# Kernel optimization log

Measured on AMD Instinct MI355X. Metric: run time of the kernel, lower is better.

The kernel has to match this reference:

```python
import jax, jax.numpy as jnp
import numpy as np

N, D, C, TOPK = 4096, 512, 512, 5


def setup_inputs() -> dict:
    key = jax.random.key(0)
    k1, k2, k3, k4 = jax.random.split(key, 4)
    feat1 = jax.random.normal(k1, (N, D), dtype=jnp.float32)
    feat2 = jax.random.normal(k2, (N, D), dtype=jnp.float32)
    # probs are softmax outputs in the original pipeline -> valid BCE inputs in (0,1)
    prob1 = jax.nn.softmax(jax.random.normal(k3, (N, C), dtype=jnp.float32), axis=-1)
    prob2 = jax.nn.softmax(jax.random.normal(k4, (N, C), dtype=jnp.float32), axis=-1)
    return {"feat1": feat1, "feat2": feat2, "prob1": prob1, "prob2": prob2, "topk": TOPK}


def reference(feat1, feat2, prob1, prob2, topk):
    # rank statistics on detached feat1: top-k feature indices, sorted as a set
    rank_idx = jnp.argsort(-feat1, axis=1)           # descending argsort, (N, D)
    top = jnp.sort(rank_idx[:, :topk], axis=1)       # (N, K) sorted top-k index sets
    # pair_enum layout: pair k = j*N + i with x1 -> row i (fast), x2 -> row j (slow).
    # Build the equivalent (N, N) matrices with rows=j, cols=i.
    rank_diff = jnp.abs(top[None, :, :] - top[:, None, :]).sum(-1)  # (N, N)
    target = (rank_diff == 0).astype(prob1.dtype)
    # pred_sim[k] = dot(prob1[i], prob2[j])  ->  P[j, i]
    pred_sim = prob2 @ prob1.T                        # (N, N)
    # BCELoss with torch's log clamp at -100
    log_p = jnp.clip(jnp.log(pred_sim), -100.0)
    log_1mp = jnp.clip(jnp.log(1.0 - pred_sim), -100.0)
    loss = -jnp.mean(target * log_p + (1.0 - target) * log_1mp)
    return loss
```

## Files before the change

### kernel.cpp

```cpp
#include <hip/hip_runtime.h>
#include <hip/hip_bf16.h>
#include <stdint.h>

#define NROWS 4096
#define CDIM  512
#define TOPK  5
#define BMJ   128
#define BNI   256
#define BK    32
#define NKT   16

typedef __bf16 bf16x8 __attribute__((ext_vector_type(8)));
typedef float  f32x4  __attribute__((ext_vector_type(4)));
typedef unsigned long long u64;

__global__ __launch_bounds__(256) void
prep_kernel(const float* __restrict__ p1, const float* __restrict__ p2,
            const float* __restrict__ feat1,
            __bf16* __restrict__ o1, __bf16* __restrict__ o2,
            u64* __restrict__ keys) {
  const int bid = blockIdx.x, tid = threadIdx.x;
  if (bid < 2048) {
    const int arr = bid >> 10;
    const int b2  = bid & 1023;
    const int kt  = b2 >> 6;
    const int c   = (b2 & 63) * 256 + tid;
    const int row = c >> 2;
    const int s   = c & 3;
    const float* src = (arr ? p2 : p1) + (size_t)row * CDIM + kt * 32 + s * 8;
    __bf16*      dst = (arr ? o2 : o1) + ((size_t)kt * NROWS + row) * 32 + ((s ^ (row & 3)) * 8);
    const float4 a = *(const float4*)src;
    const float4 b = *(const float4*)(src + 4);
    bf16x8 v;
    v[0]=(__bf16)a.x; v[1]=(__bf16)a.y; v[2]=(__bf16)a.z; v[3]=(__bf16)a.w;
    v[4]=(__bf16)b.x; v[5]=(__bf16)b.y; v[6]=(__bf16)b.z; v[7]=(__bf16)b.w;
    *(bf16x8*)dst = v;
  } else {
    const int row = (bid - 2048) * 4 + (tid >> 6);
    const int l   = tid & 63;
    const float* r = feat1 + (size_t)row * CDIM;
    float v[8];
    const float4 a = *(const float4*)(r + l * 8);
    const float4 b = *(const float4*)(r + l * 8 + 4);
    v[0]=a.x; v[1]=a.y; v[2]=a.z; v[3]=a.w;
    v[4]=b.x; v[5]=b.y; v[6]=b.z; v[7]=b.w;

    int sel[TOPK];
#pragma unroll
    for (int s = 0; s < TOPK; ++s) {
      float bv = -__builtin_inff();
      int   bi = 0x7fffffff;
#pragma unroll
      for (int t = 0; t < 8; ++t)
        if (v[t] > bv) { bv = v[t]; bi = l * 8 + t; }
#pragma unroll
      for (int off = 32; off > 0; off >>= 1) {
        float ov = __shfl_xor(bv, off);
        int   oi = __shfl_xor(bi, off);
        if (ov > bv || (ov == bv && oi < bi)) { bv = ov; bi = oi; }
      }
      sel[s] = bi;
      const int loc = bi - l * 8;
      if (loc >= 0 && loc < 8) v[loc] = -__builtin_inff();
    }
#define CSWAP(x, y) { int mn = min(sel[x], sel[y]); int mx = max(sel[x], sel[y]); sel[x] = mn; sel[y] = mx; }
    CSWAP(0,1) CSWAP(3,4) CSWAP(2,4) CSWAP(2,3) CSWAP(1,4)
    CSWAP(0,3) CSWAP(0,2) CSWAP(1,3) CSWAP(1,2)
#undef CSWAP
    if (l == 0) {
      keys[row] = (u64)sel[0] | ((u64)sel[1] << 9) | ((u64)sel[2] << 18)
                | ((u64)sel[3] << 27) | ((u64)sel[4] << 36);
    }
  }
}

__global__ __launch_bounds__(512, 4) void
gemm_loss_kernel(const __bf16* __restrict__ o1k,
                 const __bf16* __restrict__ o2k,
                 const u64* __restrict__ keys,
                 float* __restrict__ partials) {
  __shared__ __bf16 smA[3][BMJ * BK];
  __shared__ __bf16 smB[3][BNI * BK];
  __shared__ float  red[512];

  const int tid = threadIdx.x;
  const int l   = tid & 63, w = tid >> 6;
  const int wr  = w >> 2,  wc = w & 3;
  const int lr  = l & 15,  kq = l >> 4;

  const int bid = blockIdx.x;
  const int x   = bid & 7, v = bid >> 3;
  const int jt  = (x & 3) * 8 + (v & 7);
  const int it  = (x >> 2) * 8 + (v >> 3);
  const int jb  = jt * BMJ, ib = it * BNI;

  f32x4 acc[4][4] = {};

  const __bf16* gA0 = o2k + (size_t)jb * 32;
  const __bf16* gB0 = o1k + (size_t)ib * 32;

  auto stage = [&](int slot, int kt) {
    const size_t ko = (size_t)kt * NROWS * 32;
    __builtin_amdgcn_global_load_lds(
        (const __attribute__((address_space(1))) unsigned int*)(const void*)(gA0 + ko + tid * 8),
        (__attribute__((address_space(3))) unsigned int*)(void*)&smA[slot][w * 512], 16, 0, 0);
#pragma unroll
    for (int i = 0; i < 2; ++i) {
      __builtin_amdgcn_global_load_lds(
          (const __attribute__((address_space(1))) unsigned int*)(const void*)(gB0 + ko + (i * 512 + tid) * 8),
          (__attribute__((address_space(3))) unsigned int*)(void*)&smB[slot][i * 4096 + w * 512], 16, 0, 0);
    }
  };

  auto compute = [&](int slot) {
    bf16x8 af[4], bfr[4];
#pragma unroll
    for (int m = 0; m < 4; ++m) {
      const int r = wr * 64 + m * 16 + lr;
      const int p = kq ^ (r & 3);
      af[m] = *(const bf16x8*)&smA[slot][r * 32 + p * 8];
    }
#pragma unroll
    for (int n = 0; n < 4; ++n) {
      const int r = wc * 64 + n * 16 + lr;
      const int p = kq ^ (r & 3);
      bfr[n] = *(const bf16x8*)&smB[slot][r * 32 + p * 8];
    }
    __builtin_amdgcn_s_setprio(1);
#pragma unroll
    for (int m = 0; m < 4; ++m)
#pragma unroll
      for (int n = 0; n < 4; ++n)
        acc[m][n] = __builtin_amdgcn_mfma_f32_16x16x32_bf16(af[m], bfr[n], acc[m][n], 0, 0, 0);
    __builtin_amdgcn_s_setprio(0);
  };

  stage(0, 0);
  stage(1, 1);
  for (int kt = 0; kt < NKT; ++kt) {
    if (kt == NKT - 1) asm volatile("s_waitcnt vmcnt(0)" ::: "memory");
    else               asm volatile("s_waitcnt vmcnt(3)" ::: "memory");
    __builtin_amdgcn_s_barrier();
    __builtin_amdgcn_sched_barrier(0);
    if (kt + 2 < NKT) stage((kt + 2) % 3, kt + 2);
    compute(kt % 3);
  }

  u64 ki[4];
#pragma unroll
  for (int n = 0; n < 4; ++n)
    ki[n] = keys[ib + wc * 64 + n * 16 + lr];

  float sum = 0.f;
#pragma unroll
  for (int m = 0; m < 4; ++m)
#pragma unroll
    for (int r = 0; r < 4; ++r) {
      const u64 kj = keys[jb + wr * 64 + m * 16 + kq * 4 + r];
#pragma unroll
      for (int n = 0; n < 4; ++n) {
        const float p = acc[m][n][r];
        const bool  t = (kj == ki[n]);
        const float xx = t ? p : (1.0f - p);
        sum += fmaxf(__logf(xx), -100.0f);
      }
    }

  red[tid] = sum;
  __syncthreads();
#pragma unroll
  for (int s = 256; s > 0; s >>= 1) {
    if (tid < s) red[tid] += red[tid + s];
    __syncthreads();
  }
  if (tid == 0) partials[bid] = red[0];
}

__global__ void finalize_kernel(const float* __restrict__ partials,
                                float* __restrict__ out) {
  __shared__ float red[256];
  red[threadIdx.x] = partials[threadIdx.x] + partials[threadIdx.x + 256];
  __syncthreads();
  for (int st = 128; st > 0; st >>= 1) {
    if (threadIdx.x < st) red[threadIdx.x] += red[threadIdx.x + st];
    __syncthreads();
  }
  if (threadIdx.x == 0) out[0] = -red[0] * (1.0f / 16777216.0f);
}

extern "C" void kernel_launch(void* const* d_in, const int* in_sizes, int n_in,
                              void* d_out, int out_size, void* d_ws, size_t ws_size,
                              hipStream_t stream) {
  (void)in_sizes; (void)n_in; (void)out_size; (void)ws_size;
  const float* feat1 = (const float*)d_in[0];
  const float* prob1 = (const float*)d_in[2];
  const float* prob2 = (const float*)d_in[3];

  __bf16* o1 = (__bf16*)d_ws;
  __bf16* o2 = (__bf16*)((char*)d_ws + (size_t)NROWS * CDIM * 2);
  u64*   keys = (u64*)((char*)d_ws + (size_t)NROWS * CDIM * 4);
  float* partials = (float*)((char*)d_ws + (size_t)NROWS * CDIM * 4 + NROWS * 8);

  prep_kernel<<<3072, 256, 0, stream>>>(prob1, prob2, feat1, o1, o2, keys);
  gemm_loss_kernel<<<512, 512, 0, stream>>>(o1, o2, keys, partials);
  finalize_kernel<<<1, 256, 0, stream>>>(partials, (float*)d_out);
}
```

Measured before the change: 40.13 us.

## Enlarge GEMM tile to 256x256 with 4-stage split-phase pipeline

Grows the output tile per block from 128x256 to 256x256, halving the grid to 256 blocks so each block gets more reuse per loaded K-slice. The K loop becomes two half-phases, with the A and B prefetches interleaved between MFMA groups across a 4-slot LDS ring. The LDS swizzle is changed to mix higher row bits. The trade-off is twice the accumulator registers, occupancy cut to 2 blocks per CU, and only 256 blocks on a 256-CU device, which risks a single under-filled wave.

```diff
diff --git a/kernel.cpp b/kernel.cpp
--- a/kernel.cpp
+++ b/kernel.cpp
@@ -5,14 +5,15 @@
 #define NROWS 4096
 #define CDIM  512
 #define TOPK  5
-#define BMJ   128
-#define BNI   256
+#define BT    256
 #define BK    32
 #define NKT   16
 
 typedef __bf16 bf16x8 __attribute__((ext_vector_type(8)));
 typedef float  f32x4  __attribute__((ext_vector_type(4)));
 typedef unsigned long long u64;
+
+__device__ __forceinline__ int swz(int row) { return (row ^ (row >> 2)) & 3; }
 
 __global__ __launch_bounds__(256) void
 prep_kernel(const float* __restrict__ p1, const float* __restrict__ p2,
@@ -28,7 +29,7 @@
     const int row = c >> 2;
     const int s   = c & 3;
     const float* src = (arr ? p2 : p1) + (size_t)row * CDIM + kt * 32 + s * 8;
-    __bf16*      dst = (arr ? o2 : o1) + ((size_t)kt * NROWS + row) * 32 + ((s ^ (row & 3)) * 8);
+    __bf16*      dst = (arr ? o2 : o1) + ((size_t)kt * NROWS + row) * 32 + ((s ^ swz(row)) * 8);
     const float4 a = *(const float4*)src;
     const float4 b = *(const float4*)(src + 4);
     bf16x8 v;
@@ -74,13 +75,13 @@
   }
 }
 
-__global__ __launch_bounds__(512, 4) void
+__global__ __launch_bounds__(512, 2) void
 gemm_loss_kernel(const __bf16* __restrict__ o1k,
                  const __bf16* __restrict__ o2k,
                  const u64* __restrict__ keys,
                  float* __restrict__ partials) {
-  __shared__ __bf16 smA[3][BMJ * BK];
-  __shared__ __bf16 smB[3][BNI * BK];
+  __shared__ __bf16 smA[4][BT * BK];
+  __shared__ __bf16 smB[4][BT * BK];
   __shared__ float  red[512];
 
   const int tid = threadIdx.x;
@@ -89,61 +90,85 @@
   const int lr  = l & 15,  kq = l >> 4;
 
   const int bid = blockIdx.x;
-  const int x   = bid & 7, v = bid >> 3;
-  const int jt  = (x & 3) * 8 + (v & 7);
-  const int it  = (x >> 2) * 8 + (v >> 3);
-  const int jb  = jt * BMJ, ib = it * BNI;
-
-  f32x4 acc[4][4] = {};
-
-  const __bf16* gA0 = o2k + (size_t)jb * 32;
-  const __bf16* gB0 = o1k + (size_t)ib * 32;
-
-  auto stage = [&](int slot, int kt) {
-    const size_t ko = (size_t)kt * NROWS * 32;
-    __builtin_amdgcn_global_load_lds(
-        (const __attribute__((address_space(1))) unsigned int*)(const void*)(gA0 + ko + tid * 8),
-        (__attribute__((address_space(3))) unsigned int*)(void*)&smA[slot][w * 512], 16, 0, 0);
-#pragma unroll
-    for (int i = 0; i < 2; ++i) {
+  const int x   = bid & 7, bv = bid >> 3;
+  const int jt  = (x & 3) * 4 + (bv & 3);
+  const int it  = (x >> 2) * 8 + (bv >> 2);
+  const int jb  = jt * BT, ib = it * BT;
+
+  f32x4 acc[8][4] = {};
+
+  auto stageA = [&](int slot, int kt) {
+    const size_t ko = (size_t)kt * NROWS * 32 + (size_t)jb * 32;
+#pragma unroll
+    for (int r = 0; r < 2; ++r)
       __builtin_amdgcn_global_load_lds(
-          (const __attribute__((address_space(1))) unsigned int*)(const void*)(gB0 + ko + (i * 512 + tid) * 8),
-          (__attribute__((address_space(3))) unsigned int*)(void*)&smB[slot][i * 4096 + w * 512], 16, 0, 0);
-    }
+          (const __attribute__((address_space(1))) unsigned int*)(const void*)(o2k + ko + (r * 512 + tid) * 8),
+          (__attribute__((address_space(3))) unsigned int*)(void*)&smA[slot][(r * 512 + w * 64) * 8], 16, 0, 0);
   };
-
-  auto compute = [&](int slot) {
-    bf16x8 af[4], bfr[4];
-#pragma unroll
-    for (int m = 0; m < 4; ++m) {
-      const int r = wr * 64 + m * 16 + lr;
-      const int p = kq ^ (r & 3);
-      af[m] = *(const bf16x8*)&smA[slot][r * 32 + p * 8];
-    }
-#pragma unroll
-    for (int n = 0; n < 4; ++n) {
-      const int r = wc * 64 + n * 16 + lr;
-      const int p = kq ^ (r & 3);
-      bfr[n] = *(const bf16x8*)&smB[slot][r * 32 + p * 8];
-    }
-    __builtin_amdgcn_s_setprio(1);
-#pragma unroll
-    for (int m = 0; m < 4; ++m)
-#pragma unroll
-      for (int n = 0; n < 4; ++n)
-        acc[m][n] = __builtin_amdgcn_mfma_f32_16x16x32_bf16(af[m], bfr[n], acc[m][n], 0, 0, 0);
-    __builtin_amdgcn_s_setprio(0);
+  auto stageB = [&](int slot, int kt) {
+    const size_t ko = (size_t)kt * NROWS * 32 + (size_t)ib * 32;
+#pragma unroll
+    for (int r = 0; r < 2; ++r)
+      __builtin_amdgcn_global_load_lds(
+          (const __attribute__((address_space(1))) unsigned int*)(const void*)(o1k + ko + (r * 512 + tid) * 8),
+          (__attribute__((address_space(3))) unsigned int*)(void*)&smB[slot][(r * 512 + w * 64) * 8], 16, 0, 0);
   };
 
-  stage(0, 0);
-  stage(1, 1);
+  stageA(0, 0); stageB(0, 0);
+  stageA(1, 1); stageB(1, 1);
+  asm volatile("s_waitcnt vmcnt(4)" ::: "memory");
+  __builtin_amdgcn_s_barrier();
+
   for (int kt = 0; kt < NKT; ++kt) {
-    if (kt == NKT - 1) asm volatile("s_waitcnt vmcnt(0)" ::: "memory");
-    else               asm volatile("s_waitcnt vmcnt(3)" ::: "memory");
-    __builtin_amdgcn_s_barrier();
-    __builtin_amdgcn_sched_barrier(0);
-    if (kt + 2 < NKT) stage((kt + 2) % 3, kt + 2);
-    compute(kt % 3);
+    const int slot = kt & 3;
+    const int nslot = (kt + 2) & 3;
+    bf16x8 bfr[4];
+
+    {
+      bf16x8 af[4];
+#pragma unroll
+      for (int n = 0; n < 4; ++n) {
+        const int r = wc * 64 + n * 16 + lr;
+        bfr[n] = *(const bf16x8*)&smB[slot][r * 32 + (kq ^ swz(r)) * 8];
+      }
+#pragma unroll
+      for (int m = 0; m < 4; ++m) {
+        const int r = wr * 128 + m * 16 + lr;
+        af[m] = *(const bf16x8*)&smA[slot][r * 32 + (kq ^ swz(r)) * 8];
+      }
+      if (kt + 2 < NKT) stageA(nslot, kt + 2);
+      __builtin_amdgcn_s_barrier();
+      __builtin_amdgcn_s_setprio(1);
+#pragma unroll
+      for (int m = 0; m < 4; ++m)
+#pragma unroll
+        for (int n = 0; n < 4; ++n)
+          acc[m][n] = __builtin_amdgcn_mfma_f32_16x16x32_bf16(af[m], bfr[n], acc[m][n], 0, 0, 0);
+      __builtin_amdgcn_s_setprio(0);
+      __builtin_amdgcn_s_barrier();
+    }
+    {
+      bf16x8 af[4];
+#pragma unroll
+      for (int m = 0; m < 4; ++m) {
+        const int r = wr * 128 + (m + 4) * 16 + lr;
+        af[m] = *(const bf16x8*)&smA[slot][r * 32 + (kq ^ swz(r)) * 8];
+      }
+      if (kt + 2 < NKT) stageB(nslot, kt + 2);
+      __builtin_amdgcn_s_barrier();
+      __builtin_amdgcn_s_setprio(1);
+#pragma unroll
+      for (int m = 0; m < 4; ++m)
+#pragma unroll
+        for (int n = 0; n < 4; ++n)
+          acc[m + 4][n] = __builtin_amdgcn_mfma_f32_16x16x32_bf16(af[m], bfr[n], acc[m + 4][n], 0, 0, 0);
+      __builtin_amdgcn_s_setprio(0);
+      if (kt < NKT - 1) {
+        if (kt == NKT - 2) asm volatile("s_waitcnt vmcnt(0)" ::: "memory");
+        else               asm volatile("s_waitcnt vmcnt(4)" ::: "memory");
+        __builtin_amdgcn_s_barrier();
+      }
+    }
   }
 
   u64 ki[4];
@@ -153,10 +178,10 @@
 
   float sum = 0.f;
 #pragma unroll
-  for (int m = 0; m < 4; ++m)
+  for (int m = 0; m < 8; ++m)
 #pragma unroll
     for (int r = 0; r < 4; ++r) {
-      const u64 kj = keys[jb + wr * 64 + m * 16 + kq * 4 + r];
+      const u64 kj = keys[jb + wr * 128 + m * 16 + kq * 4 + r];
 #pragma unroll
       for (int n = 0; n < 4; ++n) {
         const float p = acc[m][n][r];
@@ -179,7 +204,7 @@
 __global__ void finalize_kernel(const float* __restrict__ partials,
                                 float* __restrict__ out) {
   __shared__ float red[256];
-  red[threadIdx.x] = partials[threadIdx.x] + partials[threadIdx.x + 256];
+  red[threadIdx.x] = partials[threadIdx.x];
   __syncthreads();
   for (int st = 128; st > 0; st >>= 1) {
     if (threadIdx.x < st) red[threadIdx.x] += red[threadIdx.x + st];
@@ -202,6 +227,6 @@
   float* partials = (float*)((char*)d_ws + (size_t)NROWS * CDIM * 4 + NROWS * 8);
 
   prep_kernel<<<3072, 256, 0, stream>>>(prob1, prob2, feat1, o1, o2, keys);
-  gemm_loss_kernel<<<512, 512, 0, stream>>>(o1, o2, keys, partials);
+  gemm_loss_kernel<<<256, 512, 0, stream>>>(o1, o2, keys, partials);
   finalize_kernel<<<1, 256, 0, stream>>>(partials, (float*)d_out);
 }
```

Measured after the change: 43.13 us. 7.5% more time.

## Fuse finalize into GEMM via last-block atomic, change LDS swizzle, use nontemporal access

Applied to the files above, without the earlier changes.

Drops the separate finalize kernel: each GEMM block writes its partial, bumps a global counter, and the last block to finish reduces all partials and writes the loss. The counter is reset inside prep_kernel, which saves one kernel launch and the gap between launches. The LDS swizzle changes from row&3 to (row^(row>>2))&3 to spread bank conflicts differently. Prep loads and stores become nontemporal. The cost is a fence plus an atomic in every block, and the result now depends on the counter reset being ordered before the GEMM kernel runs.

```diff
diff --git a/kernel.cpp b/kernel.cpp
--- a/kernel.cpp
+++ b/kernel.cpp
@@ -9,17 +9,22 @@
 #define BNI   256
 #define BK    32
 #define NKT   16
+#define NBLK  512
 
 typedef __bf16 bf16x8 __attribute__((ext_vector_type(8)));
 typedef float  f32x4  __attribute__((ext_vector_type(4)));
+typedef unsigned u32x4 __attribute__((ext_vector_type(4)));
 typedef unsigned long long u64;
+
+__device__ __forceinline__ int swz(int row) { return (row ^ (row >> 2)) & 3; }
 
 __global__ __launch_bounds__(256) void
 prep_kernel(const float* __restrict__ p1, const float* __restrict__ p2,
             const float* __restrict__ feat1,
             __bf16* __restrict__ o1, __bf16* __restrict__ o2,
-            u64* __restrict__ keys) {
+            u64* __restrict__ keys, unsigned* __restrict__ counter) {
   const int bid = blockIdx.x, tid = threadIdx.x;
+  if (bid == 0 && tid == 0) *counter = 0;
   if (bid < 2048) {
     const int arr = bid >> 10;
     const int b2  = bid & 1023;
@@ -28,22 +33,24 @@
     const int row = c >> 2;
     const int s   = c & 3;
     const float* src = (arr ? p2 : p1) + (size_t)row * CDIM + kt * 32 + s * 8;
-    __bf16*      dst = (arr ? o2 : o1) + ((size_t)kt * NROWS + row) * 32 + ((s ^ (row & 3)) * 8);
-    const float4 a = *(const float4*)src;
-    const float4 b = *(const float4*)(src + 4);
+    __bf16*      dst = (arr ? o2 : o1) + ((size_t)kt * NROWS + row) * 32 + ((s ^ swz(row)) * 8);
+    const f32x4 a = __builtin_nontemporal_load((const f32x4*)src);
+    const f32x4 b = __builtin_nontemporal_load((const f32x4*)(src + 4));
     bf16x8 v;
-    v[0]=(__bf16)a.x; v[1]=(__bf16)a.y; v[2]=(__bf16)a.z; v[3]=(__bf16)a.w;
-    v[4]=(__bf16)b.x; v[5]=(__bf16)b.y; v[6]=(__bf16)b.z; v[7]=(__bf16)b.w;
-    *(bf16x8*)dst = v;
+    v[0]=(__bf16)a[0]; v[1]=(__bf16)a[1]; v[2]=(__bf16)a[2]; v[3]=(__bf16)a[3];
+    v[4]=(__bf16)b[0]; v[5]=(__bf16)b[1]; v[6]=(__bf16)b[2]; v[7]=(__bf16)b[3];
+    u32x4 bits;
+    __builtin_memcpy(&bits, &v, 16);
+    __builtin_nontemporal_store(bits, (u32x4*)dst);
   } else {
     const int row = (bid - 2048) * 4 + (tid >> 6);
     const int l   = tid & 63;
     const float* r = feat1 + (size_t)row * CDIM;
     float v[8];
-    const float4 a = *(const float4*)(r + l * 8);
-    const float4 b = *(const float4*)(r + l * 8 + 4);
-    v[0]=a.x; v[1]=a.y; v[2]=a.z; v[3]=a.w;
-    v[4]=b.x; v[5]=b.y; v[6]=b.z; v[7]=b.w;
+    const f32x4 a = __builtin_nontemporal_load((const f32x4*)(r + l * 8));
+    const f32x4 b = __builtin_nontemporal_load((const f32x4*)(r + l * 8 + 4));
+    v[0]=a[0]; v[1]=a[1]; v[2]=a[2]; v[3]=a[3];
+    v[4]=b[0]; v[5]=b[1]; v[6]=b[2]; v[7]=b[3];
 
     int sel[TOPK];
 #pragma unroll
@@ -78,10 +85,13 @@
 gemm_loss_kernel(const __bf16* __restrict__ o1k,
                  const __bf16* __restrict__ o2k,
                  const u64* __restrict__ keys,
-                 float* __restrict__ partials) {
+                 float* __restrict__ partials,
+                 unsigned* __restrict__ counter,
+                 float* __restrict__ out) {
   __shared__ __bf16 smA[3][BMJ * BK];
   __shared__ __bf16 smB[3][BNI * BK];
   __shared__ float  red[512];
+  __shared__ int    lastflag;
 
   const int tid = threadIdx.x;
   const int l   = tid & 63, w = tid >> 6;
@@ -117,14 +127,12 @@
 #pragma unroll
     for (int m = 0; m < 4; ++m) {
       const int r = wr * 64 + m * 16 + lr;
-      const int p = kq ^ (r & 3);
-      af[m] = *(const bf16x8*)&smA[slot][r * 32 + p * 8];
+      af[m] = *(const bf16x8*)&smA[slot][r * 32 + (kq ^ swz(r)) * 8];
     }
 #pragma unroll
     for (int n = 0; n < 4; ++n) {
       const int r = wc * 64 + n * 16 + lr;
-      const int p = kq ^ (r & 3);
-      bfr[n] = *(const bf16x8*)&smB[slot][r * 32 + p * 8];
+      bfr[n] = *(const bf16x8*)&smB[slot][r * 32 + (kq ^ swz(r)) * 8];
     }
     __builtin_amdgcn_s_setprio(1);
 #pragma unroll
@@ -173,19 +181,23 @@
     if (tid < s) red[tid] += red[tid + s];
     __syncthreads();
   }
-  if (tid == 0) partials[bid] = red[0];
-}
-
-__global__ void finalize_kernel(const float* __restrict__ partials,
-                                float* __restrict__ out) {
-  __shared__ float red[256];
-  red[threadIdx.x] = partials[threadIdx.x] + partials[threadIdx.x + 256];
+  if (tid == 0) {
+    partials[bid] = red[0];
+    __threadfence();
+    lastflag = (atomicAdd(counter, 1u) == NBLK - 1u);
+    if (lastflag) __threadfence();
+  }
   __syncthreads();
-  for (int st = 128; st > 0; st >>= 1) {
-    if (threadIdx.x < st) red[threadIdx.x] += red[threadIdx.x + st];
+  if (lastflag) {
+    red[tid] = partials[tid];
     __syncthreads();
-  }
-  if (threadIdx.x == 0) out[0] = -red[0] * (1.0f / 16777216.0f);
+#pragma unroll
+    for (int s = 256; s > 0; s >>= 1) {
+      if (tid < s) red[tid] += red[tid + s];
+      __syncthreads();
+    }
+    if (tid == 0) out[0] = -red[0] * (1.0f / 16777216.0f);
+  }
 }
 
 extern "C" void kernel_launch(void* const* d_in, const int* in_sizes, int n_in,
@@ -200,8 +212,8 @@
   __bf16* o2 = (__bf16*)((char*)d_ws + (size_t)NROWS * CDIM * 2);
   u64*   keys = (u64*)((char*)d_ws + (size_t)NROWS * CDIM * 4);
   float* partials = (float*)((char*)d_ws + (size_t)NROWS * CDIM * 4 + NROWS * 8);
-
-  prep_kernel<<<3072, 256, 0, stream>>>(prob1, prob2, feat1, o1, o2, keys);
-  gemm_loss_kernel<<<512, 512, 0, stream>>>(o1, o2, keys, partials);
-  finalize_kernel<<<1, 256, 0, stream>>>(partials, (float*)d_out);
+  unsigned* counter = (unsigned*)((char*)d_ws + (size_t)NROWS * CDIM * 4 + NROWS * 8 + NBLK * 4);
+
+  prep_kernel<<<3072, 256, 0, stream>>>(prob1, prob2, feat1, o1, o2, keys, counter);
+  gemm_loss_kernel<<<NBLK, 512, 0, stream>>>(o1, o2, keys, partials, counter, (float*)d_out);
 }
```

Result: slower. 48.06 us (+19.7%).
